# Performance work log

Measured on AMD Instinct MI355X. Metric: run time of the kernel, lower is better.

## Reference

```python
import jax, jax.numpy as jnp
import numpy as np
import math

B_ = 4
L_ = 2048
D_MODEL = 1024
D_STATE = 128
D_CONV = 4
HEADDIM = 64
CHUNK = 256
D_INNER = 2 * D_MODEL
NHEADS = D_INNER // HEADDIM
CONV_DIM = D_INNER + 2 * D_STATE
D_IN_PROJ = 2 * D_INNER + 2 * D_STATE + NHEADS


def setup_inputs() -> dict:
    key = jax.random.key(0)
    ks = jax.random.split(key, 8)
    u = jax.random.normal(ks[0], (B_, L_, D_MODEL), jnp.float32)
    W_in = jax.random.normal(ks[1], (D_IN_PROJ, D_MODEL), jnp.float32) * 0.02
    conv_w = jax.random.normal(ks[2], (CONV_DIM, D_CONV), jnp.float32) * 0.2
    conv_b = jnp.zeros((CONV_DIM,), jnp.float32)
    # dt init as in the torch module: dt ~ logU(0.001, 0.1), inverse-softplus
    dt = jnp.exp(jax.random.uniform(ks[3], (NHEADS,), jnp.float32) * (math.log(0.1) - math.log(0.001)) + math.log(0.001))
    dt = jnp.clip(dt, 1e-4, None)
    dt_bias = dt + jnp.log(-jnp.expm1(-dt))
    A_log = jnp.log(jax.random.uniform(ks[4], (NHEADS,), jnp.float32, minval=1.0, maxval=1.1))
    D_param = jnp.ones((NHEADS,), jnp.float32)
    norm_w = jnp.ones((D_INNER,), jnp.float32)
    W_out = jax.random.normal(ks[5], (D_MODEL, D_INNER), jnp.float32) * 0.02
    return {"u": u, "W_in": W_in, "conv_w": conv_w, "conv_b": conv_b,
            "dt_bias": dt_bias, "A_log": A_log, "D_param": D_param,
            "norm_w": norm_w, "W_out": W_out}


def _ssd(x, dt, A, Bm, Cm):
    """Chunked SSD scan (mamba_chunk_scan_combined math, ngroups=1).
    x: (b,l,h,p)  dt: (b,l,h) post-softplus  A: (h,)  Bm/Cm: (b,l,n)."""
    b, l, h, p = x.shape
    n = Bm.shape[-1]
    nc = l // CHUNK
    xr = x.reshape(b, nc, CHUNK, h, p)
    dtr = dt.reshape(b, nc, CHUNK, h)
    Br = Bm.reshape(b, nc, CHUNK, n)
    Cr = Cm.reshape(b, nc, CHUNK, n)
    dA = dtr * A                                    # (b,nc,cs,h), negative
    dA_cs = jnp.cumsum(dA, axis=2)                  # (b,nc,cs,h)
    # intra-chunk decay L[i,j] = exp(sum_{k=j+1..i} dA_k) for i >= j else 0
    diff = dA_cs[:, :, :, None, :] - dA_cs[:, :, None, :, :]  # (b,nc,i,j,h)
    mask = jnp.tril(jnp.ones((CHUNK, CHUNK), bool))
    Lmat = jnp.exp(jnp.where(mask[None, None, :, :, None], diff, -jnp.inf))
    dtx = dtr[..., None] * xr                       # (b,nc,cs,h,p)
    Y_diag = jnp.einsum('bcin,bcjn,bcijh,bcjhp->bcihp', Cr, Br, Lmat, dtx)
    # per-chunk final states
    decay_states = jnp.exp(dA_cs[:, :, -1:, :] - dA_cs)  # (b,nc,cs,h)
    states = jnp.einsum('bcjn,bcjh,bcjhp->bchpn', Br, decay_states, dtx)
    # inter-chunk recurrence over nc
    chunk_decay = jnp.exp(dA_cs[:, :, -1, :])       # (b,nc,h)
    def step(carry, inp):
        s, d = inp
        return carry * d[:, :, None, None] + s, carry
    init = jnp.zeros((b, h, p, n), x.dtype)
    _, prev = jax.lax.scan(step, init, (jnp.moveaxis(states, 1, 0), jnp.moveaxis(chunk_decay, 1, 0)))
    prev = jnp.moveaxis(prev, 0, 1)                 # (b,nc,h,p,n): state entering each chunk
    Y_off = jnp.einsum('bcin,bchpn,bcih->bcihp', Cr, prev, jnp.exp(dA_cs))
    return (Y_diag + Y_off).reshape(b, l, h, p)


def reference(u, W_in, conv_w, conv_b, dt_bias, A_log, D_param, norm_w, W_out):
    b, l, _ = u.shape
    zxbcdt = jnp.einsum('bld,ed->ble', u, W_in)     # (b,l,d_in_proj)
    z = zxbcdt[..., :D_INNER]
    xBC = zxbcdt[..., D_INNER:D_INNER + CONV_DIM]
    dt = zxbcdt[..., D_INNER + CONV_DIM:]
    # depthwise causal conv1d + SiLU
    xt = jnp.moveaxis(xBC, 1, 2)                    # (b,c,l)
    y = jax.lax.conv_general_dilated(xt, conv_w[:, None, :], (1,), [(D_CONV - 1, 0)], feature_group_count=CONV_DIM)
    xBC = jax.nn.silu(jnp.moveaxis(y + conv_b[None, :, None], 2, 1))
    x = xBC[..., :D_INNER].reshape(b, l, NHEADS, HEADDIM)
    Bm = xBC[..., D_INNER:D_INNER + D_STATE]
    Cm = xBC[..., D_INNER + D_STATE:]
    dt = jax.nn.softplus(dt + dt_bias)
    A = -jnp.exp(A_log)
    yh = _ssd(x, dt, A, Bm, Cm) + D_param[:, None] * x
    yf = yh.reshape(b, l, D_INNER)
    # gated RMSNorm (norm_before_gate=False): norm(y * silu(z)) * w
    g = yf * jax.nn.silu(z)
    g = g * jax.lax.rsqrt(jnp.mean(g * g, axis=-1, keepdims=True) + 1e-5) * norm_w
    return jnp.einsum('bld,ed->ble', g, W_out)
```

## Files before the change

### kernel.cpp

```cpp
#include <hip/hip_runtime.h>
#include <hip/hip_bf16.h>
#include <math.h>

#define B_N     4
#define L_N     2048
#define DMODEL  1024
#define DSTATE  128
#define DCONV   4
#define HEADDIM 64
#define CHUNK   256
#define DINNER  2048
#define NHEADS  32
#define CONVDIM 2304
#define DINPROJ 4384
#define NCHUNK  8
#define BL      (B_N*L_N)

typedef unsigned short ushort_t;
typedef unsigned int   uint_t;

typedef __attribute__((ext_vector_type(8))) short bf16x8;
typedef __attribute__((ext_vector_type(4))) float f32x4;

__device__ __forceinline__ float bfbits2f(ushort_t u){
    union { uint_t i; float f; } v; v.i = ((uint_t)u) << 16; return v.f;
}
__device__ __forceinline__ ushort_t f2bf(float f){
    union { float f; uint_t i; } v; v.f = f;
    uint_t r = v.i + 0x7FFF + ((v.i >> 16) & 1);
    return (ushort_t)(r >> 16);
}
__device__ __forceinline__ void gload_lds16(const void* g, void* l){
    __builtin_amdgcn_global_load_lds(
        (const __attribute__((address_space(1))) unsigned int*)g,
        (__attribute__((address_space(3))) unsigned int*)l, 16, 0, 0);
}

#define N_U8  (BL*DMODEL/8)
#define N_WI8 (DINPROJ*DMODEL/8)
#define N_WO8 (DMODEL*DINNER/8)

__global__ __launch_bounds__(256) void cvt_all(
    const float* __restrict__ u, const float* __restrict__ W_in,
    const float* __restrict__ W_out,
    ushort_t* __restrict__ u_bf, ushort_t* __restrict__ Wi_bf,
    ushort_t* __restrict__ Wo_bf)
{
    int i = blockIdx.x*256 + threadIdx.x;
    const float* src; ushort_t* dst; int off;
    if (i < N_U8)                { src = u;     dst = u_bf;  off = i; }
    else if (i < N_U8+N_WI8)     { src = W_in;  dst = Wi_bf; off = i - N_U8; }
    else if (i < N_U8+N_WI8+N_WO8){ src = W_out; dst = Wo_bf; off = i - N_U8 - N_WI8; }
    else return;
    const float4* p = (const float4*)(src + (size_t)off*8);
    float4 a = p[0], b = p[1];
    ushort_t o[8] = { f2bf(a.x), f2bf(a.y), f2bf(a.z), f2bf(a.w),
                      f2bf(b.x), f2bf(b.y), f2bf(b.z), f2bf(b.w) };
    *(uint4*)(dst + (size_t)off*8) = *(const uint4*)o;
}

__global__ __launch_bounds__(256) void cvt_wT(
    const float* __restrict__ cw, float* __restrict__ wT)
{
    int c = blockIdx.x*256 + threadIdx.x;
    if (c >= CONVDIM) return;
    float4 v = *(const float4*)&cw[c*DCONV];
    wT[0*CONVDIM + c] = v.x;
    wT[1*CONVDIM + c] = v.y;
    wT[2*CONVDIM + c] = v.z;
    wT[3*CONVDIM + c] = v.w;
}

template<int KDIM, int NTILES, int EPI>
__global__ __launch_bounds__(256) void gemm_bt_mfma(
    const ushort_t* __restrict__ A, const ushort_t* __restrict__ B,
    float* __restrict__ outf, ushort_t* __restrict__ z, ushort_t* __restrict__ xbc,
    const float* __restrict__ dt_bias, float* __restrict__ dtp)
{
    __shared__ __align__(16) ushort_t Asl[2][128*32];
    __shared__ __align__(16) ushort_t Bsl[2][128*32];

    int nwg = gridDim.x, cpx = nwg >> 3, lin = blockIdx.x;
    int work = (lin & 7)*cpx + (lin >> 3);
    int mtile = work / NTILES, ntile = work % NTILES;
    int m0 = mtile*128, n0 = ntile*128;

    int t = threadIdx.x;
    int l = t & 63, w = t >> 6;
    int wr = w >> 1, wc = w & 1;
    int lr16 = l & 15, kb = l >> 4;
    int srow = t >> 2, skc = (t & 3)*8;

    f32x4 acc[4][4];
    #pragma unroll
    for (int m=0;m<4;m++){
        #pragma unroll
        for (int n=0;n<4;n++) acc[m][n] = (f32x4){0.f,0.f,0.f,0.f};
    }

    int br0 = n0 + srow, br1 = n0 + 64 + srow;
    if (EPI == 1){
        br0 = (br0 < DINPROJ) ? br0 : (DINPROJ-1);
        br1 = (br1 < DINPROJ) ? br1 : (DINPROJ-1);
    }

    auto stage = [&](int buf, int k0){
        gload_lds16(A + (size_t)(m0+srow)*KDIM + k0 + skc,    &Asl[buf][t*8]);
        gload_lds16(A + (size_t)(m0+64+srow)*KDIM + k0 + skc, &Asl[buf][2048 + t*8]);
        gload_lds16(B + (size_t)br0*KDIM + k0 + skc,          &Bsl[buf][t*8]);
        gload_lds16(B + (size_t)br1*KDIM + k0 + skc,          &Bsl[buf][2048 + t*8]);
    };

    auto compute = [&](int cur){
        bf16x8 af[4], bfr[4];
        #pragma unroll
        for (int m=0;m<4;m++) af[m]  = *(const bf16x8*)&Asl[cur][(wr*64+m*16+lr16)*32 + kb*8];
        #pragma unroll
        for (int n=0;n<4;n++) bfr[n] = *(const bf16x8*)&Bsl[cur][(wc*64+n*16+lr16)*32 + kb*8];
        __builtin_amdgcn_s_setprio(1);
        #pragma unroll
        for (int m=0;m<4;m++){
            #pragma unroll
            for (int n=0;n<4;n++)
                acc[m][n] = __builtin_amdgcn_mfma_f32_16x16x32_bf16(af[m], bfr[n], acc[m][n], 0, 0, 0);
        }
        __builtin_amdgcn_s_setprio(0);
    };

    stage(0, 0);
    __syncthreads();
    int cur = 0;
    for (int k0=32; k0<KDIM; k0+=32){
        stage(cur^1, k0);
        compute(cur);
        __syncthreads();
        cur ^= 1;
    }
    compute(cur);

    #pragma unroll
    for (int m=0;m<4;m++){
        int rbase = m0 + wr*64 + m*16 + (l>>4)*4;
        #pragma unroll
        for (int n=0;n<4;n++){
            int gcol = n0 + wc*64 + n*16 + lr16;
            f32x4 v = acc[m][n];
            #pragma unroll
            for (int q=0;q<4;q++){
                int row = rbase + q;
                if (EPI == 0) {
                    outf[(size_t)row*DMODEL + gcol] = v[q];
                } else {
                    if (gcol < DINNER) {
                        z[(size_t)row*DINNER + gcol] = f2bf(v[q]);
                    } else if (gcol < DINNER + CONVDIM) {
                        xbc[(size_t)row*CONVDIM + (gcol - DINNER)] = f2bf(v[q]);
                    } else if (gcol < DINPROJ) {
                        int hh = gcol - (DINNER + CONVDIM);
                        float x = v[q] + dt_bias[hh];
                        float sp = (x > 15.f) ? x : log1pf(__expf(x));
                        int bb = row >> 11, ll = row & (L_N-1);
                        dtp[((size_t)bb*NHEADS + hh)*L_N + ll] = sp;
                    }
                }
            }
        }
    }
}

__global__ __launch_bounds__(256) void conv_silu(
    const __hip_bfloat16* __restrict__ xraw,
    const float* __restrict__ wT, const float* __restrict__ cb,
    __hip_bfloat16* __restrict__ xout)
{
    int idx = blockIdx.x*256 + threadIdx.x;
    int c8 = (idx % (CONVDIM/8))*8;
    int ml = idx / (CONVDIM/8);
    int b  = ml / (L_N/2);
    int l  = (ml % (L_N/2))*2;
    const ushort_t* xr = (const ushort_t*)xraw;

    float wv[4][8];
    #pragma unroll
    for (int k=0;k<DCONV;k++){
        float4 w0 = *(const float4*)&wT[k*CONVDIM + c8];
        float4 w1 = *(const float4*)&wT[k*CONVDIM + c8 + 4];
        wv[k][0]=w0.x; wv[k][1]=w0.y; wv[k][2]=w0.z; wv[k][3]=w0.w;
        wv[k][4]=w1.x; wv[k][5]=w1.y; wv[k][6]=w1.z; wv[k][7]=w1.w;
    }
    float bias[8];
    {
        float4 b0 = *(const float4*)&cb[c8];
        float4 b1 = *(const float4*)&cb[c8+4];
        bias[0]=b0.x; bias[1]=b0.y; bias[2]=b0.z; bias[3]=b0.w;
        bias[4]=b1.x; bias[5]=b1.y; bias[6]=b1.z; bias[7]=b1.w;
    }

    float xv[5][8];
    #pragma unroll
    for (int r=0;r<5;r++){
        int li = l - 3 + r;
        if (li >= 0){
            bf16x8 v = *(const bf16x8*)&xr[((size_t)b*L_N + li)*CONVDIM + c8];
            #pragma unroll
            for (int e=0;e<8;e++) xv[r][e] = bfbits2f(((const ushort_t*)&v)[e]);
        } else {
            #pragma unroll
            for (int e=0;e<8;e++) xv[r][e] = 0.f;
        }
    }

    ushort_t o0[8], o1[8];
    #pragma unroll
    for (int e=0;e<8;e++){
        float a0 = bias[e], a1 = bias[e];
        #pragma unroll
        for (int k=0;k<DCONV;k++){
            a0 += wv[k][e]*xv[k][e];
            a1 += wv[k][e]*xv[k+1][e];
        }
        o0[e] = f2bf(a0 / (1.f + __expf(-a0)));
        o1[e] = f2bf(a1 / (1.f + __expf(-a1)));
    }
    ushort_t* ob = (ushort_t*)xout + ((size_t)b*L_N + l)*CONVDIM + c8;
    *(uint4*)ob = *(const uint4*)o0;
    *(uint4*)(ob + CONVDIM) = *(const uint4*)o1;
}

__global__ __launch_bounds__(256) void dt_cumsum(
    const float* __restrict__ dtp, const float* __restrict__ A_log,
    float* __restrict__ dAcs)
{
    int blk = blockIdx.x;
    int c  = blk % NCHUNK;
    int bh = blk / NCHUNK;
    int h  = bh & (NHEADS-1);
    int t  = threadIdx.x;
    float A = -__expf(A_log[h]);
    __shared__ float sm[CHUNK];
    float v = dtp[(size_t)bh*L_N + c*CHUNK + t] * A;
    sm[t] = v;
    __syncthreads();
    for (int off=1; off<CHUNK; off<<=1){
        float add = (t >= off) ? sm[t-off] : 0.f;
        __syncthreads();
        sm[t] += add;
        __syncthreads();
    }
    dAcs[(size_t)bh*L_N + c*CHUNK + t] = sm[t];
}

__global__ __launch_bounds__(256) void bc_scores_mfma(
    const __hip_bfloat16* __restrict__ xbc, ushort_t* __restrict__ S_T)
{
    __shared__ __align__(16) ushort_t Bs2[256*136];
    __shared__ __align__(16) ushort_t Cs2[256*136];
    int bc = blockIdx.x;
    int t = threadIdx.x;
    int l = t & 63, w = t >> 6;
    int l15 = l & 15, l4 = l >> 4;
    const ushort_t* xb = (const ushort_t*)xbc;
    const size_t rowbase = (size_t)bc*CHUNK*CONVDIM;

    #pragma unroll
    for (int ps=0; ps<16; ps++){
        int idx = ps*256 + t;
        int r = idx >> 4, ck = idx & 15;
        *(uint4*)&Bs2[r*136 + ck*8] =
            *(const uint4*)&xb[rowbase + (size_t)r*CONVDIM + DINNER + ck*8];
        *(uint4*)&Cs2[r*136 + ck*8] =
            *(const uint4*)&xb[rowbase + (size_t)r*CONVDIM + (DINNER+DSTATE) + ck*8];
    }
    __syncthreads();

    ushort_t* Sb = S_T + (size_t)bc*CHUNK*264;
    for (int if4 = w; if4 < 4; if4++){
        f32x4 acc[4][4];
        #pragma unroll
        for (int jf=0;jf<4;jf++){
            #pragma unroll
            for (int ir=0;ir<4;ir++) acc[jf][ir] = (f32x4){0.f,0.f,0.f,0.f};
        }
        #pragma unroll
        for (int k=0;k<4;k++){
            bf16x8 af[4], bfC[4];
            #pragma unroll
            for (int jf=0;jf<4;jf++)
                af[jf] = *(const bf16x8*)&Bs2[(w*64 + jf*16 + l15)*136 + k*32 + l4*8];
            #pragma unroll
            for (int ir=0;ir<4;ir++)
                bfC[ir] = *(const bf16x8*)&Cs2[(if4*64 + ir*16 + l15)*136 + k*32 + l4*8];
            #pragma unroll
            for (int jf=0;jf<4;jf++){
                #pragma unroll
                for (int ir=0;ir<4;ir++)
                    acc[jf][ir] = __builtin_amdgcn_mfma_f32_16x16x32_bf16(af[jf], bfC[ir], acc[jf][ir], 0, 0, 0);
            }
        }
        #pragma unroll
        for (int jf=0;jf<4;jf++){
            #pragma unroll
            for (int ir=0;ir<4;ir++){
                #pragma unroll
                for (int q=0;q<4;q++){
                    int j = w*64 + jf*16 + l4*4 + q;
                    int i = if4*64 + ir*16 + l15;
                    Sb[(size_t)j*264 + i] = f2bf(acc[jf][ir][q]);
                }
            }
        }
    }
}

__device__ __forceinline__ int swz264(int row, int col){
    return row*264 + (col ^ (((row>>3)&7)<<3));
}

__global__ __launch_bounds__(256) void ssd_states_mfma(
    const __hip_bfloat16* __restrict__ xbc,
    const float* __restrict__ dtp, const float* __restrict__ dAcs,
    float* __restrict__ states)
{
    __shared__ __align__(16) ushort_t xdT[64*264];
    __shared__ __align__(16) ushort_t BT[128*264];
    __shared__ float coef_s[CHUNK];
    int bc = blockIdx.x, hg = blockIdx.y;
    int b = bc >> 3, c = bc & 7;
    int t = threadIdx.x;
    int l = t & 63, w = t >> 6;
    int l15 = l & 15, l4 = l >> 4;
    const ushort_t* xb = (const ushort_t*)xbc;
    const size_t rowbase = (size_t)bc*CHUNK*CONVDIM;

    #pragma unroll
    for (int ps=0; ps<16; ps++){
        int idx = ps*256 + t;
        int j = idx >> 4, n0 = (idx & 15)*8;
        bf16x8 v = *(const bf16x8*)&xb[rowbase + (size_t)j*CONVDIM + DINNER + n0];
        #pragma unroll
        for (int e=0;e<8;e++)
            BT[swz264(n0+e, j)] = ((const ushort_t*)&v)[e];
    }

    for (int hh=0; hh<4; hh++){
        int h = hg*4 + hh;
        size_t dbase = ((size_t)b*NHEADS + h)*L_N + c*CHUNK;
        float last = dAcs[dbase + CHUNK-1];
        float cf = __expf(last - dAcs[dbase + t]) * dtp[dbase + t];
        coef_s[t] = cf;
        __syncthreads();

        #pragma unroll
        for (int ps=0; ps<8; ps++){
            int idx = ps*256 + t;
            int j = idx >> 3, p0 = (idx & 7)*8;
            float cj = coef_s[j];
            bf16x8 v = *(const bf16x8*)&xb[rowbase + (size_t)j*CONVDIM + h*HEADDIM + p0];
            #pragma unroll
            for (int e=0;e<8;e++)
                xdT[swz264(p0+e, j)] = f2bf(cj * bfbits2f(((const ushort_t*)&v)[e]));
        }
        __syncthreads();

        f32x4 acc[4][2];
        #pragma unroll
        for (int pf=0;pf<4;pf++){
            #pragma unroll
            for (int nf=0;nf<2;nf++) acc[pf][nf] = (f32x4){0.f,0.f,0.f,0.f};
        }

        #pragma unroll
        for (int k=0;k<8;k++){
            bf16x8 af[4], bv[2];
            #pragma unroll
            for (int pf=0;pf<4;pf++)
                af[pf] = *(const bf16x8*)&xdT[swz264(pf*16 + l15, k*32 + l4*8)];
            #pragma unroll
            for (int nf=0;nf<2;nf++)
                bv[nf] = *(const bf16x8*)&BT[swz264(w*32 + nf*16 + l15, k*32 + l4*8)];
            __builtin_amdgcn_s_setprio(1);
            #pragma unroll
            for (int pf=0;pf<4;pf++){
                #pragma unroll
                for (int nf=0;nf<2;nf++)
                    acc[pf][nf] = __builtin_amdgcn_mfma_f32_16x16x32_bf16(af[pf], bv[nf], acc[pf][nf], 0, 0, 0);
            }
            __builtin_amdgcn_s_setprio(0);
        }

        float* sb = states + (size_t)(bc*NHEADS + h)*HEADDIM*DSTATE;
        #pragma unroll
        for (int pf=0;pf<4;pf++){
            #pragma unroll
            for (int nf=0;nf<2;nf++){
                #pragma unroll
                for (int q=0;q<4;q++){
                    int p = pf*16 + l4*4 + q;
                    int n = w*32 + nf*16 + l15;
                    sb[(size_t)p*DSTATE + n] = acc[pf][nf][q];
                }
            }
        }
    }
}

__global__ __launch_bounds__(256) void scan_states(
    const float* __restrict__ states, const float* __restrict__ dAcs,
    ushort_t* __restrict__ prev_bf)
{
    int idx = blockIdx.x*256 + threadIdx.x;
    int n  = idx & 127;
    int p  = (idx >> 7) & 63;
    int bh = idx >> 13;
    int b  = bh >> 5, h = bh & 31;
    float carry = 0.f;
    for (int c=0;c<NCHUNK;c++){
        size_t off = (((size_t)((b*NCHUNK + c)*NHEADS + h))*HEADDIM + p)*DSTATE + n;
        prev_bf[off] = f2bf(carry);
        float s = states[off];
        float cd = __expf(dAcs[((size_t)b*NHEADS + h)*L_N + c*CHUNK + (CHUNK-1)]);
        carry = carry * cd + s;
    }
}

__global__ __launch_bounds__(256) void ssd_mfma(
    const __hip_bfloat16* __restrict__ xbc,
    const float* __restrict__ dtp, const float* __restrict__ dAcs,
    const ushort_t* __restrict__ prev_bf, const ushort_t* __restrict__ S_T,
    const float* __restrict__ D_param, ushort_t* __restrict__ yh)
{
    __shared__ __align__(16) ushort_t Ws[256*72];
    __shared__ __align__(16) ushort_t xdT[64*264];
    __shared__ float da_s[CHUNK];
    __shared__ float dt_s[CHUNK];

    int bc = blockIdx.x, h = blockIdx.y;
    int b = bc >> 3, c = bc & 7;
    int t = threadIdx.x;
    int l = t & 63, w = t >> 6;
    int l15 = l & 15, l4 = l >> 4;

    const ushort_t* xb = (const ushort_t*)xbc;
    const size_t rowbase = (size_t)bc*CHUNK*CONVDIM;

    da_s[t] = dAcs[((size_t)b*NHEADS + h)*L_N + c*CHUNK + t];
    dt_s[t] = dtp[((size_t)b*NHEADS + h)*L_N + c*CHUNK + t];

    #pragma unroll
    for (int ps=0; ps<8; ps++){
        int idx = ps*256 + t;
        int j = idx >> 3, p0 = (idx & 7)*8;
        bf16x8 v = *(const bf16x8*)&xb[rowbase + (size_t)j*CONVDIM + h*HEADDIM + p0];
        #pragma unroll
        for (int e=0;e<8;e++) xdT[(p0+e)*264 + j] = ((const ushort_t*)&v)[e];
    }
    __syncthreads();

    f32x4 yacc[4][4];
    #pragma unroll
    for (int m=0;m<4;m++){
        #pragma unroll
        for (int np=0;np<4;np++) yacc[m][np] = (f32x4){0.f,0.f,0.f,0.f};
    }

    const ushort_t* cbase = xb + rowbase + (size_t)l15*CONVDIM + (DINNER+DSTATE) + l4*8;
    const ushort_t* pbase = prev_bf + (size_t)(bc*NHEADS + h)*HEADDIM*DSTATE
                                    + (size_t)l15*DSTATE + l4*8;
    #pragma unroll
    for (int k=0;k<4;k++){
        bf16x8 bfk[4];
        #pragma unroll
        for (int np=0;np<4;np++)
            bfk[np] = *(const bf16x8*)(pbase + (size_t)(np*16)*DSTATE + k*32);
        bf16x8 af0 = *(const bf16x8*)(cbase + (size_t)((0*4+w)*16)*CONVDIM + k*32);
        bf16x8 af1 = *(const bf16x8*)(cbase + (size_t)((1*4+w)*16)*CONVDIM + k*32);
        bf16x8 af2 = *(const bf16x8*)(cbase + (size_t)((2*4+w)*16)*CONVDIM + k*32);
        bf16x8 af3 = *(const bf16x8*)(cbase + (size_t)((3*4+w)*16)*CONVDIM + k*32);
        __builtin_amdgcn_s_setprio(1);
        #pragma unroll
        for (int np=0;np<4;np++){
            yacc[0][np] = __builtin_amdgcn_mfma_f32_16x16x32_bf16(af0, bfk[np], yacc[0][np], 0, 0, 0);
            yacc[1][np] = __builtin_amdgcn_mfma_f32_16x16x32_bf16(af1, bfk[np], yacc[1][np], 0, 0, 0);
            yacc[2][np] = __builtin_amdgcn_mfma_f32_16x16x32_bf16(af2, bfk[np], yacc[2][np], 0, 0, 0);
            yacc[3][np] = __builtin_amdgcn_mfma_f32_16x16x32_bf16(af3, bfk[np], yacc[3][np], 0, 0, 0);
        }
        __builtin_amdgcn_s_setprio(0);
    }
    #pragma unroll
    for (int m=0;m<4;m++){
        int i0 = (m*4 + w)*16;
        #pragma unroll
        for (int q=0;q<4;q++){
            float e = __expf(da_s[i0 + l4*4 + q]);
            #pragma unroll
            for (int np=0;np<4;np++) yacc[m][np][q] *= e;
        }
    }

    const ushort_t* Sb = S_T + (size_t)bc*CHUNK*264;
    for (int jp=0; jp<4; jp++){
        bf16x8 bfx[4][2];
        #pragma unroll
        for (int np=0;np<4;np++){
            #pragma unroll
            for (int ks=0;ks<2;ks++)
                bfx[np][ks] = *(const bf16x8*)&xdT[(np*16 + l15)*264 + jp*64 + ks*32 + l4*8];
        }

        #pragma unroll
        for (int m=0;m<4;m++){
            int i0 = (m*4 + w)*16;
            int imax = i0 + 15;
            int kmaxY = (jp*64 <= imax ? 1 : 0) + (jp*64+32 <= imax ? 1 : 0);
            if (kmaxY == 0) continue;
            int nmax = 2*kmaxY;

            float dai[4];
            #pragma unroll
            for (int q=0;q<4;q++) dai[q] = da_s[i0 + l4*4 + q];
            #pragma unroll
            for (int n=0;n<4;n++){
                if (n < nmax){
                    int jcol = jp*64 + n*16 + l15;
                    float daj = da_s[jcol], dtj = dt_s[jcol];
                    ushort_t sv[4];
                    *(uint2*)sv = *(const uint2*)&Sb[(size_t)jcol*264 + i0 + l4*4];
                    #pragma unroll
                    for (int q=0;q<4;q++){
                        int i = i0 + l4*4 + q;
                        float wv = 0.f;
                        if (jcol <= i) wv = __expf(dai[q] - daj) * dtj * bfbits2f(sv[q]);
                        Ws[i*72 + n*16 + l15] = f2bf(wv);
                    }
                }
            }
            __builtin_amdgcn_s_setprio(1);
            #pragma unroll
            for (int ks=0;ks<2;ks++){
                if (ks < kmaxY){
                    bf16x8 wfA = *(const bf16x8*)&Ws[(i0 + l15)*72 + ks*32 + l4*8];
                    #pragma unroll
                    for (int np=0;np<4;np++)
                        yacc[m][np] = __builtin_amdgcn_mfma_f32_16x16x32_bf16(wfA, bfx[np][ks], yacc[m][np], 0, 0, 0);
                }
            }
            __builtin_amdgcn_s_setprio(0);
        }
    }

    float Dh = D_param[h];
    #pragma unroll
    for (int m=0;m<4;m++){
        int i0 = (m*4 + w)*16;
        #pragma unroll
        for (int np=0;np<4;np++){
            int p = np*16 + l15;
            #pragma unroll
            for (int q=0;q<4;q++){
                int i = i0 + l4*4 + q;
                float xv = bfbits2f(xdT[p*264 + i]);
                yh[((size_t)bc*CHUNK + i)*DINNER + h*HEADDIM + p] = f2bf(yacc[m][np][q] + Dh*xv);
            }
        }
    }
}

__global__ __launch_bounds__(256) void gate_norm(
    const ushort_t* __restrict__ yh, const __hip_bfloat16* __restrict__ z,
    const float* __restrict__ norm_w, __hip_bfloat16* __restrict__ g)
{
    int row = blockIdx.x;
    int t = threadIdx.x;
    const ushort_t* yr = yh + (size_t)row*DINNER + t*8;
    const ushort_t* zr = (const ushort_t*)z + (size_t)row*DINNER + t*8;
    bf16x8 yv = *(const bf16x8*)yr;
    bf16x8 zv8 = *(const bf16x8*)zr;
    float v[8];
    float ss = 0.f;
    #pragma unroll
    for (int e=0;e<8;e++){
        float y = bfbits2f(((const ushort_t*)&yv)[e]);
        float zz = bfbits2f(((const ushort_t*)&zv8)[e]);
        float gv = y * (zz / (1.f + __expf(-zz)));
        v[e] = gv; ss += gv*gv;
    }
    #pragma unroll
    for (int off=32; off>=1; off>>=1) ss += __shfl_xor(ss, off);
    __shared__ float red[4];
    if ((t & 63) == 0) red[t >> 6] = ss;
    __syncthreads();
    float tot = red[0]+red[1]+red[2]+red[3];
    float scale = rsqrtf(tot * (1.f/DINNER) + 1e-5f);
    float4 w0 = *(const float4*)&norm_w[t*8];
    float4 w1 = *(const float4*)&norm_w[t*8+4];
    float nw[8] = {w0.x,w0.y,w0.z,w0.w,w1.x,w1.y,w1.z,w1.w};
    ushort_t o[8];
    #pragma unroll
    for (int e=0;e<8;e++) o[e] = f2bf(v[e]*scale*nw[e]);
    *(uint4*)((ushort_t*)g + (size_t)row*DINNER + t*8) = *(const uint4*)o;
}

extern "C" void kernel_launch(void* const* d_in, const int* in_sizes, int n_in,
                              void* d_out, int out_size, void* d_ws, size_t ws_size,
                              hipStream_t stream)
{
    const float* u       = (const float*)d_in[0];
    const float* W_in    = (const float*)d_in[1];
    const float* conv_w  = (const float*)d_in[2];
    const float* conv_b  = (const float*)d_in[3];
    const float* dt_bias = (const float*)d_in[4];
    const float* A_log   = (const float*)d_in[5];
    const float* D_param = (const float*)d_in[6];
    const float* norm_w  = (const float*)d_in[7];
    const float* W_out   = (const float*)d_in[8];
    float* out = (float*)d_out;

    char* p = (char*)d_ws;
    auto take = [&](size_t n){ char* r = p; p += (n + 255) & ~(size_t)255; return r; };

    __hip_bfloat16* z       = (__hip_bfloat16*)take((size_t)BL*DINNER*2);
    __hip_bfloat16* xbc_raw = (__hip_bfloat16*)take((size_t)BL*CONVDIM*2);
    __hip_bfloat16* xbc     = (__hip_bfloat16*)take((size_t)BL*CONVDIM*2);
    float* dtp     = (float*)take((size_t)BL*NHEADS*4);
    float* dAcs    = (float*)take((size_t)BL*NHEADS*4);
    float* states  = (float*)take((size_t)B_N*NCHUNK*NHEADS*HEADDIM*DSTATE*4);
    ushort_t* prev_bf = (ushort_t*)take((size_t)B_N*NCHUNK*NHEADS*HEADDIM*DSTATE*2);
    ushort_t* yh   = (ushort_t*)take((size_t)BL*DINNER*2);
    ushort_t* S_T  = (ushort_t*)take((size_t)B_N*NCHUNK*CHUNK*264*2);
    ushort_t* u_bf  = (ushort_t*)take((size_t)BL*DMODEL*2);
    ushort_t* Wi_bf = (ushort_t*)take((size_t)DINPROJ*DMODEL*2);
    ushort_t* Wo_bf = (ushort_t*)take((size_t)DMODEL*DINNER*2);
    float* wT       = (float*)take((size_t)DCONV*CONVDIM*4);
    __hip_bfloat16* g = z;

    cvt_all<<<dim3((N_U8+N_WI8+N_WO8 + 255)/256), 256, 0, stream>>>(
        u, W_in, W_out, u_bf, Wi_bf, Wo_bf);
    cvt_wT<<<dim3((CONVDIM+255)/256), 256, 0, stream>>>(conv_w, wT);

    gemm_bt_mfma<DMODEL,35,1><<<dim3(64*35), 256, 0, stream>>>(
        u_bf, Wi_bf, nullptr, (ushort_t*)z, (ushort_t*)xbc_raw, dt_bias, dtp);

    conv_silu<<<dim3((BL/2)*(CONVDIM/8)/256), 256, 0, stream>>>(xbc_raw, wT, conv_b, xbc);
    dt_cumsum<<<dim3(B_N*NHEADS*NCHUNK), 256, 0, stream>>>(dtp, A_log, dAcs);
    bc_scores_mfma<<<dim3(B_N*NCHUNK), 256, 0, stream>>>(xbc, S_T);
    ssd_states_mfma<<<dim3(B_N*NCHUNK, NHEADS/4), 256, 0, stream>>>(xbc, dtp, dAcs, states);
    scan_states<<<dim3((B_N*NHEADS*HEADDIM*DSTATE)/256), 256, 0, stream>>>(states, dAcs, prev_bf);
    ssd_mfma<<<dim3(B_N*NCHUNK, NHEADS), 256, 0, stream>>>(xbc, dtp, dAcs, prev_bf, S_T, D_param, yh);
    gate_norm<<<dim3(BL), 256, 0, stream>>>(yh, z, norm_w, g);

    gemm_bt_mfma<DINNER,8,0><<<dim3(64*8), 256, 0, stream>>>(
        (const ushort_t*)g, Wo_bf, out, nullptr, nullptr, nullptr, nullptr);
}
```

Baseline: 352.5 us.

## Split bc_scores and ssd_states across more blocks for higher occupancy

bc_scores_mfma now launches one block per chunk and 64-column C tile (4x grid), so each block loads only its C slice and does a single tile per wave. Waves whose tile lies above the diagonal exit early. ssd_states_mfma splits the 128-wide state dimension into two halves across blockIdx.y, which doubles the grid to 512 blocks and halves the B tile in shared memory. The aim is to fill more compute units and raise occupancy in kernels that previously had only 32 or 256 blocks. The cost is redundant loads of B and x across the split blocks.

After: 348.2 us. No clear change (-1.2%).

```diff
diff --git a/kernel.cpp b/kernel.cpp
--- a/kernel.cpp
+++ b/kernel.cpp
@@ -254,8 +254,8 @@
     const __hip_bfloat16* __restrict__ xbc, ushort_t* __restrict__ S_T)
 {
     __shared__ __align__(16) ushort_t Bs2[256*136];
-    __shared__ __align__(16) ushort_t Cs2[256*136];
-    int bc = blockIdx.x;
+    __shared__ __align__(16) ushort_t Cs2[64*136];
+    int bc = blockIdx.x, if4 = blockIdx.y;
     int t = threadIdx.x;
     int l = t & 63, w = t >> 6;
     int l15 = l & 15, l4 = l >> 4;
@@ -268,45 +268,50 @@
         int r = idx >> 4, ck = idx & 15;
         *(uint4*)&Bs2[r*136 + ck*8] =
             *(const uint4*)&xb[rowbase + (size_t)r*CONVDIM + DINNER + ck*8];
+    }
+    #pragma unroll
+    for (int ps=0; ps<4; ps++){
+        int idx = ps*256 + t;
+        int r = idx >> 4, ck = idx & 15;
         *(uint4*)&Cs2[r*136 + ck*8] =
-            *(const uint4*)&xb[rowbase + (size_t)r*CONVDIM + (DINNER+DSTATE) + ck*8];
+            *(const uint4*)&xb[rowbase + (size_t)(if4*64 + r)*CONVDIM + (DINNER+DSTATE) + ck*8];
     }
     __syncthreads();
 
+    if (w > if4) return;
+
+    f32x4 acc[4][4];
+    #pragma unroll
+    for (int jf=0;jf<4;jf++){
+        #pragma unroll
+        for (int ir=0;ir<4;ir++) acc[jf][ir] = (f32x4){0.f,0.f,0.f,0.f};
+    }
+    #pragma unroll
+    for (int k=0;k<4;k++){
+        bf16x8 af[4], bfC[4];
+        #pragma unroll
+        for (int jf=0;jf<4;jf++)
+            af[jf] = *(const bf16x8*)&Bs2[(w*64 + jf*16 + l15)*136 + k*32 + l4*8];
+        #pragma unroll
+        for (int ir=0;ir<4;ir++)
+            bfC[ir] = *(const bf16x8*)&Cs2[(ir*16 + l15)*136 + k*32 + l4*8];
+        #pragma unroll
+        for (int jf=0;jf<4;jf++){
+            #pragma unroll
+            for (int ir=0;ir<4;ir++)
+                acc[jf][ir] = __builtin_amdgcn_mfma_f32_16x16x32_bf16(af[jf], bfC[ir], acc[jf][ir], 0, 0, 0);
+        }
+    }
     ushort_t* Sb = S_T + (size_t)bc*CHUNK*264;
-    for (int if4 = w; if4 < 4; if4++){
-        f32x4 acc[4][4];
-        #pragma unroll
-        for (int jf=0;jf<4;jf++){
-            #pragma unroll
-            for (int ir=0;ir<4;ir++) acc[jf][ir] = (f32x4){0.f,0.f,0.f,0.f};
-        }
-        #pragma unroll
-        for (int k=0;k<4;k++){
-            bf16x8 af[4], bfC[4];
-            #pragma unroll
-            for (int jf=0;jf<4;jf++)
-                af[jf] = *(const bf16x8*)&Bs2[(w*64 + jf*16 + l15)*136 + k*32 + l4*8];
-            #pragma unroll
-            for (int ir=0;ir<4;ir++)
-                bfC[ir] = *(const bf16x8*)&Cs2[(if4*64 + ir*16 + l15)*136 + k*32 + l4*8];
-            #pragma unroll
-            for (int jf=0;jf<4;jf++){
-                #pragma unroll
-                for (int ir=0;ir<4;ir++)
-                    acc[jf][ir] = __builtin_amdgcn_mfma_f32_16x16x32_bf16(af[jf], bfC[ir], acc[jf][ir], 0, 0, 0);
-            }
-        }
-        #pragma unroll
-        for (int jf=0;jf<4;jf++){
-            #pragma unroll
-            for (int ir=0;ir<4;ir++){
-                #pragma unroll
-                for (int q=0;q<4;q++){
-                    int j = w*64 + jf*16 + l4*4 + q;
-                    int i = if4*64 + ir*16 + l15;
-                    Sb[(size_t)j*264 + i] = f2bf(acc[jf][ir][q]);
-                }
+    #pragma unroll
+    for (int jf=0;jf<4;jf++){
+        #pragma unroll
+        for (int ir=0;ir<4;ir++){
+            #pragma unroll
+            for (int q=0;q<4;q++){
+                int j = w*64 + jf*16 + l4*4 + q;
+                int i = if4*64 + ir*16 + l15;
+                Sb[(size_t)j*264 + i] = f2bf(acc[jf][ir][q]);
             }
         }
     }
@@ -322,9 +327,10 @@
     float* __restrict__ states)
 {
     __shared__ __align__(16) ushort_t xdT[64*264];
-    __shared__ __align__(16) ushort_t BT[128*264];
+    __shared__ __align__(16) ushort_t BTh[64*264];
     __shared__ float coef_s[CHUNK];
-    int bc = blockIdx.x, hg = blockIdx.y;
+    int bc = blockIdx.x;
+    int hg = blockIdx.y >> 1, nh = blockIdx.y & 1;
     int b = bc >> 3, c = bc & 7;
     int t = threadIdx.x;
     int l = t & 63, w = t >> 6;
@@ -333,13 +339,13 @@
     const size_t rowbase = (size_t)bc*CHUNK*CONVDIM;
 
     #pragma unroll
-    for (int ps=0; ps<16; ps++){
+    for (int ps=0; ps<8; ps++){
         int idx = ps*256 + t;
-        int j = idx >> 4, n0 = (idx & 15)*8;
-        bf16x8 v = *(const bf16x8*)&xb[rowbase + (size_t)j*CONVDIM + DINNER + n0];
+        int j = idx >> 3, n0 = (idx & 7)*8;
+        bf16x8 v = *(const bf16x8*)&xb[rowbase + (size_t)j*CONVDIM + DINNER + nh*64 + n0];
         #pragma unroll
         for (int e=0;e<8;e++)
-            BT[swz264(n0+e, j)] = ((const ushort_t*)&v)[e];
+            BTh[swz264(n0+e, j)] = ((const ushort_t*)&v)[e];
     }
 
     for (int hh=0; hh<4; hh++){
@@ -362,43 +368,32 @@
         }
         __syncthreads();
 
-        f32x4 acc[4][2];
-        #pragma unroll
-        for (int pf=0;pf<4;pf++){
-            #pragma unroll
-            for (int nf=0;nf<2;nf++) acc[pf][nf] = (f32x4){0.f,0.f,0.f,0.f};
-        }
+        f32x4 acc[4];
+        #pragma unroll
+        for (int pf=0;pf<4;pf++) acc[pf] = (f32x4){0.f,0.f,0.f,0.f};
 
         #pragma unroll
         for (int k=0;k<8;k++){
-            bf16x8 af[4], bv[2];
+            bf16x8 af[4];
             #pragma unroll
             for (int pf=0;pf<4;pf++)
                 af[pf] = *(const bf16x8*)&xdT[swz264(pf*16 + l15, k*32 + l4*8)];
-            #pragma unroll
-            for (int nf=0;nf<2;nf++)
-                bv[nf] = *(const bf16x8*)&BT[swz264(w*32 + nf*16 + l15, k*32 + l4*8)];
+            bf16x8 bv = *(const bf16x8*)&BTh[swz264(w*16 + l15, k*32 + l4*8)];
             __builtin_amdgcn_s_setprio(1);
             #pragma unroll
-            for (int pf=0;pf<4;pf++){
-                #pragma unroll
-                for (int nf=0;nf<2;nf++)
-                    acc[pf][nf] = __builtin_amdgcn_mfma_f32_16x16x32_bf16(af[pf], bv[nf], acc[pf][nf], 0, 0, 0);
-            }
+            for (int pf=0;pf<4;pf++)
+                acc[pf] = __builtin_amdgcn_mfma_f32_16x16x32_bf16(af[pf], bv, acc[pf], 0, 0, 0);
             __builtin_amdgcn_s_setprio(0);
         }
 
         float* sb = states + (size_t)(bc*NHEADS + h)*HEADDIM*DSTATE;
+        int n = nh*64 + w*16 + l15;
         #pragma unroll
         for (int pf=0;pf<4;pf++){
             #pragma unroll
-            for (int nf=0;nf<2;nf++){
-                #pragma unroll
-                for (int q=0;q<4;q++){
-                    int p = pf*16 + l4*4 + q;
-                    int n = w*32 + nf*16 + l15;
-                    sb[(size_t)p*DSTATE + n] = acc[pf][nf][q];
-                }
+            for (int q=0;q<4;q++){
+                int p = pf*16 + l4*4 + q;
+                sb[(size_t)p*DSTATE + n] = acc[pf][q];
             }
         }
     }
@@ -642,8 +637,8 @@
 
     conv_silu<<<dim3((BL/2)*(CONVDIM/8)/256), 256, 0, stream>>>(xbc_raw, wT, conv_b, xbc);
     dt_cumsum<<<dim3(B_N*NHEADS*NCHUNK), 256, 0, stream>>>(dtp, A_log, dAcs);
-    bc_scores_mfma<<<dim3(B_N*NCHUNK), 256, 0, stream>>>(xbc, S_T);
-    ssd_states_mfma<<<dim3(B_N*NCHUNK, NHEADS/4), 256, 0, stream>>>(xbc, dtp, dAcs, states);
+    bc_scores_mfma<<<dim3(B_N*NCHUNK, 4), 256, 0, stream>>>(xbc, S_T);
+    ssd_states_mfma<<<dim3(B_N*NCHUNK, 16), 256, 0, stream>>>(xbc, dtp, dAcs, states);
     scan_states<<<dim3((B_N*NHEADS*HEADDIM*DSTATE)/256), 256, 0, stream>>>(states, dAcs, prev_bf);
     ssd_mfma<<<dim3(B_N*NCHUNK, NHEADS), 256, 0, stream>>>(xbc, dtp, dAcs, prev_bf, S_T, D_param, yh);
     gate_norm<<<dim3(BL), 256, 0, stream>>>(yh, z, norm_w, g);
```
